# Kernel optimization log

Measured on AMD Instinct MI355X. Metric: run time of the kernel, lower is better.

The kernel has to match this reference:

```python
import jax, jax.numpy as jnp
import numpy as np

N = 1024
IN_F = 256
OUT_F = 128
H = 4
NH = OUT_F // H  # 32
NEG_SLOPE = 0.2


def setup_inputs() -> dict:
    key = jax.random.key(0)
    k1, k2, k3, k4, k5 = jax.random.split(key, 5)
    h = jax.random.normal(k1, (N, IN_F), dtype=jnp.float32)
    adj_mat = jax.random.randint(k2, (N, N, 1), 0, 2, dtype=jnp.int32)
    s_in = 1.0 / np.sqrt(IN_F)
    s_nh = 1.0 / np.sqrt(NH)
    Wl = jax.random.uniform(k3, (H * NH, IN_F), jnp.float32, -s_in, s_in)
    Wr = jax.random.uniform(k4, (H * NH, IN_F), jnp.float32, -s_in, s_in)
    attn_w = jax.random.uniform(k5, (NH,), jnp.float32, -s_nh, s_nh)
    return {"h": h, "adj_mat": adj_mat, "Wl": Wl, "Wr": Wr, "attn_w": attn_w}


def reference(h, adj_mat, Wl, Wr, attn_w):
    n = h.shape[0]
    g_l = (h @ Wl.T).reshape(n, H, NH)  # [N,H,F]
    g_r = (h @ Wr.T).reshape(n, H, NH)  # [N,H,F]
    # g_sum[i, j] = g_l[j] + g_r[i]  (repeat / repeat_interleave semantics)
    g_sum = g_l[None, :, :, :] + g_r[:, None, :, :]  # [N,N,H,F]
    act = jnp.where(g_sum >= 0, g_sum, NEG_SLOPE * g_sum)
    e = jnp.einsum('ijhf,f->ijh', act, attn_w)  # [N,N,H]
    mask = adj_mat != 0  # [N,N,1] broadcasts over heads
    e = jnp.where(mask, e, -jnp.inf)
    a = jax.nn.softmax(e, axis=1)  # softmax over source nodes j
    h_prime = jnp.einsum('ijh,jhf->ihf', a, g_r).reshape(n, H * NH)
    # is_output_layer=False -> ELU (dropout is a no-op in eval)
    return jax.nn.elu(h_prime)
```

## Files before the change

kernel.cpp:

```cpp
#include <hip/hip_runtime.h>
#include <math.h>

#define NN 1024
#define IN_F 256
#define OUT_F 128
#define NHEADS 4
#define NHF 32

__global__ void __launch_bounds__(256) glr_gemm(const float* __restrict__ hmat,
                                                const float* __restrict__ Wl,
                                                const float* __restrict__ Wr,
                                                float* __restrict__ glh,
                                                float* __restrict__ grh) {
    __shared__ float hsh[4][IN_F];
    const int tid = threadIdx.x;
    const int j0  = blockIdx.x * 4;
    for (int t = tid; t < 4 * IN_F; t += 256) {
        hsh[t >> 8][t & 255] = hmat[j0 * IN_F + t];
    }
    __syncthreads();
    const int c = tid;
    const float* __restrict__ Wrow = (c < OUT_F) ? (Wl + c * IN_F) : (Wr + (c - OUT_F) * IN_F);
    float acc0 = 0.f, acc1 = 0.f, acc2 = 0.f, acc3 = 0.f;
#pragma unroll 4
    for (int k = 0; k < IN_F; k += 4) {
        const float4 w  = *(const float4*)(Wrow + k);
        const float4 a0 = *(const float4*)&hsh[0][k];
        const float4 a1 = *(const float4*)&hsh[1][k];
        const float4 a2 = *(const float4*)&hsh[2][k];
        const float4 a3 = *(const float4*)&hsh[3][k];
        acc0 = fmaf(a0.x, w.x, fmaf(a0.y, w.y, fmaf(a0.z, w.z, fmaf(a0.w, w.w, acc0))));
        acc1 = fmaf(a1.x, w.x, fmaf(a1.y, w.y, fmaf(a1.z, w.z, fmaf(a1.w, w.w, acc1))));
        acc2 = fmaf(a2.x, w.x, fmaf(a2.y, w.y, fmaf(a2.z, w.z, fmaf(a2.w, w.w, acc2))));
        acc3 = fmaf(a3.x, w.x, fmaf(a3.y, w.y, fmaf(a3.z, w.z, fmaf(a3.w, w.w, acc3))));
    }
    const int which = (c >= OUT_F);
    const int cc = which ? (c - OUT_F) : c;
    const int hh = cc >> 5, f = cc & 31;
    float* __restrict__ dst = which ? grh : glh;
    dst[(hh * NN + j0 + 0) * NHF + f] = acc0;
    dst[(hh * NN + j0 + 1) * NHF + f] = acc1;
    dst[(hh * NN + j0 + 2) * NHF + f] = acc2;
    dst[(hh * NN + j0 + 3) * NHF + f] = acc3;
}

__global__ void __launch_bounds__(256) gat_main(const float* __restrict__ glh,
                                                const float* __restrict__ grh,
                                                const int* __restrict__ adj,
                                                const float* __restrict__ attn_w,
                                                float* __restrict__ out) {
    const int hh  = blockIdx.y;
    const int i0  = blockIdx.x * 8;
    const int tid = threadIdx.x;

    __shared__ float e_buf[8][1028];
    __shared__ float gr_i[8][32];
    __shared__ float wred[8][4];
    __shared__ float m_sh[8];
    __shared__ float l_sh[8];

    {
        const int ii = tid >> 5, f = tid & 31;
        gr_i[ii][f] = grh[(hh * NN + i0 + ii) * NHF + f];
    }
    float w06[NHF];
#pragma unroll
    for (int f = 0; f < NHF; ++f) w06[f] = 0.6f * attn_w[f];
    const float C23 = 0x1.555556p-1f;
    __syncthreads();

    float mpart[8];
#pragma unroll
    for (int ii = 0; ii < 8; ++ii) mpart[ii] = -1e30f;

    for (int c = 0; c < 4; ++c) {
        const int j = (c << 8) + tid;
        float gl_r[NHF];
#pragma unroll
        for (int f4 = 0; f4 < 8; ++f4) {
            const float4 v = *(const float4*)(glh + (hh * NN + j) * NHF + (f4 << 2));
            gl_r[f4 * 4 + 0] = v.x; gl_r[f4 * 4 + 1] = v.y;
            gl_r[f4 * 4 + 2] = v.z; gl_r[f4 * 4 + 3] = v.w;
        }
        int adjv[8];
#pragma unroll
        for (int ii = 0; ii < 8; ++ii) adjv[ii] = adj[(i0 + ii) * NN + j];
#pragma unroll
        for (int ii = 0; ii < 8; ++ii) {
            float e = 0.f;
#pragma unroll
            for (int f4 = 0; f4 < 8; ++f4) {
                const float4 g = *(const float4*)&gr_i[ii][f4 << 2];
                float s;
                s = gl_r[f4 * 4 + 0] + g.x; e = fmaf(fmaf(fabsf(s), C23, s), w06[f4 * 4 + 0], e);
                s = gl_r[f4 * 4 + 1] + g.y; e = fmaf(fmaf(fabsf(s), C23, s), w06[f4 * 4 + 1], e);
                s = gl_r[f4 * 4 + 2] + g.z; e = fmaf(fmaf(fabsf(s), C23, s), w06[f4 * 4 + 2], e);
                s = gl_r[f4 * 4 + 3] + g.w; e = fmaf(fmaf(fabsf(s), C23, s), w06[f4 * 4 + 3], e);
            }
            e = adjv[ii] ? e : -1e30f;
            e_buf[ii][j] = e;
            mpart[ii] = fmaxf(mpart[ii], e);
        }
    }

#pragma unroll
    for (int ii = 0; ii < 8; ++ii) {
        float v = mpart[ii];
#pragma unroll
        for (int d = 32; d > 0; d >>= 1) v = fmaxf(v, __shfl_xor(v, d));
        if ((tid & 63) == 0) wred[ii][tid >> 6] = v;
    }
    __syncthreads();
    if (tid < 8) m_sh[tid] = fmaxf(fmaxf(wred[tid][0], wred[tid][1]),
                                   fmaxf(wred[tid][2], wred[tid][3]));
    __syncthreads();

    float lpart[8];
#pragma unroll
    for (int ii = 0; ii < 8; ++ii) lpart[ii] = 0.f;
    for (int c = 0; c < 4; ++c) {
        const int j = (c << 8) + tid;
#pragma unroll
        for (int ii = 0; ii < 8; ++ii) {
            const float p = __expf(e_buf[ii][j] - m_sh[ii]);
            e_buf[ii][j] = p;
            lpart[ii] += p;
        }
    }
#pragma unroll
    for (int ii = 0; ii < 8; ++ii) {
        float v = lpart[ii];
#pragma unroll
        for (int d = 32; d > 0; d >>= 1) v += __shfl_xor(v, d);
        if ((tid & 63) == 0) wred[ii][tid >> 6] = v;
    }
    __syncthreads();
    if (tid < 8) l_sh[tid] = wred[tid][0] + wred[tid][1] + wred[tid][2] + wred[tid][3];
    __syncthreads();

    const int ii = tid >> 5, f = tid & 31;
    const float* __restrict__ grb = grh + hh * NN * NHF + f;
    float o0 = 0.f, o1 = 0.f, o2 = 0.f, o3 = 0.f;
    for (int j = 0; j < NN; j += 4) {
        const float4 p4 = *(const float4*)&e_buf[ii][j];
        const float g0 = grb[(j + 0) * NHF];
        const float g1 = grb[(j + 1) * NHF];
        const float g2 = grb[(j + 2) * NHF];
        const float g3 = grb[(j + 3) * NHF];
        o0 = fmaf(p4.x, g0, o0);
        o1 = fmaf(p4.y, g1, o1);
        o2 = fmaf(p4.z, g2, o2);
        o3 = fmaf(p4.w, g3, o3);
    }
    float o = (o0 + o1) + (o2 + o3);
    o /= l_sh[ii];
    const float r = (o > 0.f) ? o : (__expf(o) - 1.f);
    out[(i0 + ii) * OUT_F + hh * NHF + f] = r;
}

extern "C" void kernel_launch(void* const* d_in, const int* in_sizes, int n_in,
                              void* d_out, int out_size, void* d_ws, size_t ws_size,
                              hipStream_t stream) {
    const float* hmat = (const float*)d_in[0];
    const int*   adj  = (const int*)d_in[1];
    const float* Wl   = (const float*)d_in[2];
    const float* Wr   = (const float*)d_in[3];
    const float* aw   = (const float*)d_in[4];
    float* o          = (float*)d_out;

    float* glh = (float*)d_ws;
    float* grh = glh + NHEADS * NN * NHF;

    glr_gemm<<<dim3(NN / 4), dim3(256), 0, stream>>>(hmat, Wl, Wr, glh, grh);
    gat_main<<<dim3(NN / 8, NHEADS), dim3(256), 0, stream>>>(glh, grh, adj, aw, o);
}
```

Measured before the change: 122.0 us.

## Split LeakyReLU into linear dot terms plus abs term, widen blocks and restructure aggregation

Leaky ReLU is rewritten as 0.6*s + 0.4*|s|, so the linear part of the attention score becomes per-node dot products (alpha, beta). These are computed in the GEMM kernel with a warp shuffle reduction, which leaves one abs-FMA per feature in the main loop. The main kernel moves to 512 threads. Aggregation now splits the j range across thread groups, each accumulating all 8 rows, then reduces partials in shared memory, which reuses each grh load for 8 rows. The GEMM processes 2 rows per block instead of 4, which doubles weight reloads, and the extra shared buffer may reduce occupancy.

```diff
diff --git a/kernel.cpp b/kernel.cpp
--- a/kernel.cpp
+++ b/kernel.cpp
@@ -10,116 +10,125 @@
 __global__ void __launch_bounds__(256) glr_gemm(const float* __restrict__ hmat,
                                                 const float* __restrict__ Wl,
                                                 const float* __restrict__ Wr,
+                                                const float* __restrict__ attn_w,
                                                 float* __restrict__ glh,
-                                                float* __restrict__ grh) {
-    __shared__ float hsh[4][IN_F];
+                                                float* __restrict__ grh,
+                                                float* __restrict__ alpha,
+                                                float* __restrict__ beta) {
+    __shared__ float hsh[2][IN_F];
     const int tid = threadIdx.x;
-    const int j0  = blockIdx.x * 4;
-    for (int t = tid; t < 4 * IN_F; t += 256) {
+    const int j0  = blockIdx.x * 2;
+    for (int t = tid; t < 2 * IN_F; t += 256) {
         hsh[t >> 8][t & 255] = hmat[j0 * IN_F + t];
     }
     __syncthreads();
     const int c = tid;
     const float* __restrict__ Wrow = (c < OUT_F) ? (Wl + c * IN_F) : (Wr + (c - OUT_F) * IN_F);
-    float acc0 = 0.f, acc1 = 0.f, acc2 = 0.f, acc3 = 0.f;
-#pragma unroll 4
+    float a0 = 0.f, a1 = 0.f;
+#pragma unroll 8
     for (int k = 0; k < IN_F; k += 4) {
         const float4 w  = *(const float4*)(Wrow + k);
-        const float4 a0 = *(const float4*)&hsh[0][k];
-        const float4 a1 = *(const float4*)&hsh[1][k];
-        const float4 a2 = *(const float4*)&hsh[2][k];
-        const float4 a3 = *(const float4*)&hsh[3][k];
-        acc0 = fmaf(a0.x, w.x, fmaf(a0.y, w.y, fmaf(a0.z, w.z, fmaf(a0.w, w.w, acc0))));
-        acc1 = fmaf(a1.x, w.x, fmaf(a1.y, w.y, fmaf(a1.z, w.z, fmaf(a1.w, w.w, acc1))));
-        acc2 = fmaf(a2.x, w.x, fmaf(a2.y, w.y, fmaf(a2.z, w.z, fmaf(a2.w, w.w, acc2))));
-        acc3 = fmaf(a3.x, w.x, fmaf(a3.y, w.y, fmaf(a3.z, w.z, fmaf(a3.w, w.w, acc3))));
+        const float4 x0 = *(const float4*)&hsh[0][k];
+        const float4 x1 = *(const float4*)&hsh[1][k];
+        a0 = fmaf(x0.x, w.x, fmaf(x0.y, w.y, fmaf(x0.z, w.z, fmaf(x0.w, w.w, a0))));
+        a1 = fmaf(x1.x, w.x, fmaf(x1.y, w.y, fmaf(x1.z, w.z, fmaf(x1.w, w.w, a1))));
+    }
+    const int f = c & 31;
+    const float wf = attn_w[f];
+    float d0 = a0 * wf, d1 = a1 * wf;
+#pragma unroll
+    for (int d = 16; d > 0; d >>= 1) {
+        d0 += __shfl_xor(d0, d);
+        d1 += __shfl_xor(d1, d);
     }
     const int which = (c >= OUT_F);
     const int cc = which ? (c - OUT_F) : c;
-    const int hh = cc >> 5, f = cc & 31;
+    const int hh = cc >> 5;
     float* __restrict__ dst = which ? grh : glh;
-    dst[(hh * NN + j0 + 0) * NHF + f] = acc0;
-    dst[(hh * NN + j0 + 1) * NHF + f] = acc1;
-    dst[(hh * NN + j0 + 2) * NHF + f] = acc2;
-    dst[(hh * NN + j0 + 3) * NHF + f] = acc3;
+    dst[(hh * NN + j0 + 0) * NHF + f] = a0;
+    dst[(hh * NN + j0 + 1) * NHF + f] = a1;
+    if (f == 0) {
+        float* __restrict__ ab = which ? beta : alpha;
+        ab[hh * NN + j0 + 0] = d0;
+        ab[hh * NN + j0 + 1] = d1;
+    }
 }
 
-__global__ void __launch_bounds__(256) gat_main(const float* __restrict__ glh,
-                                                const float* __restrict__ grh,
-                                                const int* __restrict__ adj,
-                                                const float* __restrict__ attn_w,
-                                                float* __restrict__ out) {
+__global__ void __launch_bounds__(512, 4) gat_main(const float* __restrict__ glh,
+                                                   const float* __restrict__ grh,
+                                                   const float* __restrict__ alpha,
+                                                   const float* __restrict__ beta,
+                                                   const int* __restrict__ adj,
+                                                   const float* __restrict__ attn_w,
+                                                   float* __restrict__ out) {
     const int hh  = blockIdx.y;
     const int i0  = blockIdx.x * 8;
     const int tid = threadIdx.x;
 
     __shared__ float e_buf[8][1028];
-    __shared__ float gr_i[8][32];
-    __shared__ float wred[8][4];
-    __shared__ float m_sh[8];
-    __shared__ float l_sh[8];
-
-    {
-        const int ii = tid >> 5, f = tid & 31;
-        gr_i[ii][f] = grh[(hh * NN + i0 + ii) * NHF + f];
-    }
-    float w06[NHF];
-#pragma unroll
-    for (int f = 0; f < NHF; ++f) w06[f] = 0.6f * attn_w[f];
-    const float C23 = 0x1.555556p-1f;
-    __syncthreads();
+    __shared__ float part[8][16][32];
+    __shared__ float red[8][8];
+    __shared__ float m_sh[8], l_sh[8];
 
     float mpart[8];
 #pragma unroll
     for (int ii = 0; ii < 8; ++ii) mpart[ii] = -1e30f;
 
-    for (int c = 0; c < 4; ++c) {
-        const int j = (c << 8) + tid;
-        float gl_r[NHF];
+    for (int c = 0; c < 2; ++c) {
+        const int j = (c << 9) + tid;
+        const float* __restrict__ gp = glh + (hh * NN + j) * NHF;
+        float gl[32];
 #pragma unroll
         for (int f4 = 0; f4 < 8; ++f4) {
-            const float4 v = *(const float4*)(glh + (hh * NN + j) * NHF + (f4 << 2));
-            gl_r[f4 * 4 + 0] = v.x; gl_r[f4 * 4 + 1] = v.y;
-            gl_r[f4 * 4 + 2] = v.z; gl_r[f4 * 4 + 3] = v.w;
-        }
+            const float4 v = *(const float4*)(gp + (f4 << 2));
+            gl[f4 * 4 + 0] = v.x; gl[f4 * 4 + 1] = v.y;
+            gl[f4 * 4 + 2] = v.z; gl[f4 * 4 + 3] = v.w;
+        }
+        const float aj = alpha[hh * NN + j];
         int adjv[8];
 #pragma unroll
         for (int ii = 0; ii < 8; ++ii) adjv[ii] = adj[(i0 + ii) * NN + j];
 #pragma unroll
         for (int ii = 0; ii < 8; ++ii) {
-            float e = 0.f;
-#pragma unroll
-            for (int f4 = 0; f4 < 8; ++f4) {
-                const float4 g = *(const float4*)&gr_i[ii][f4 << 2];
-                float s;
-                s = gl_r[f4 * 4 + 0] + g.x; e = fmaf(fmaf(fabsf(s), C23, s), w06[f4 * 4 + 0], e);
-                s = gl_r[f4 * 4 + 1] + g.y; e = fmaf(fmaf(fabsf(s), C23, s), w06[f4 * 4 + 1], e);
-                s = gl_r[f4 * 4 + 2] + g.z; e = fmaf(fmaf(fabsf(s), C23, s), w06[f4 * 4 + 2], e);
-                s = gl_r[f4 * 4 + 3] + g.w; e = fmaf(fmaf(fabsf(s), C23, s), w06[f4 * 4 + 3], e);
+            const float* __restrict__ grp = grh + (hh * NN + i0 + ii) * NHF;
+            float S0 = 0.f, S1 = 0.f;
+#pragma unroll
+            for (int f = 0; f < 32; f += 2) {
+                const float s0 = gl[f]     + grp[f];
+                const float s1 = gl[f + 1] + grp[f + 1];
+                S0 = fmaf(fabsf(s0), attn_w[f],     S0);
+                S1 = fmaf(fabsf(s1), attn_w[f + 1], S1);
             }
+            const float bi = beta[hh * NN + i0 + ii];
+            float e = fmaf(0.4f, S0 + S1, 0.6f * (aj + bi));
             e = adjv[ii] ? e : -1e30f;
             e_buf[ii][j] = e;
             mpart[ii] = fmaxf(mpart[ii], e);
         }
     }
 
+    const int lane = tid & 63, wv = tid >> 6;
 #pragma unroll
     for (int ii = 0; ii < 8; ++ii) {
         float v = mpart[ii];
 #pragma unroll
         for (int d = 32; d > 0; d >>= 1) v = fmaxf(v, __shfl_xor(v, d));
-        if ((tid & 63) == 0) wred[ii][tid >> 6] = v;
-    }
-    __syncthreads();
-    if (tid < 8) m_sh[tid] = fmaxf(fmaxf(wred[tid][0], wred[tid][1]),
-                                   fmaxf(wred[tid][2], wred[tid][3]));
+        if (lane == 0) red[ii][wv] = v;
+    }
+    __syncthreads();
+    if (tid < 8) {
+        float m = red[tid][0];
+#pragma unroll
+        for (int w = 1; w < 8; ++w) m = fmaxf(m, red[tid][w]);
+        m_sh[tid] = m;
+    }
     __syncthreads();
 
     float lpart[8];
 #pragma unroll
     for (int ii = 0; ii < 8; ++ii) lpart[ii] = 0.f;
-    for (int c = 0; c < 4; ++c) {
-        const int j = (c << 8) + tid;
+    for (int c = 0; c < 2; ++c) {
+        const int j = (c << 9) + tid;
 #pragma unroll
         for (int ii = 0; ii < 8; ++ii) {
             const float p = __expf(e_buf[ii][j] - m_sh[ii]);
@@ -132,30 +141,49 @@
         float v = lpart[ii];
 #pragma unroll
         for (int d = 32; d > 0; d >>= 1) v += __shfl_xor(v, d);
-        if ((tid & 63) == 0) wred[ii][tid >> 6] = v;
-    }
-    __syncthreads();
-    if (tid < 8) l_sh[tid] = wred[tid][0] + wred[tid][1] + wred[tid][2] + wred[tid][3];
-    __syncthreads();
-
-    const int ii = tid >> 5, f = tid & 31;
-    const float* __restrict__ grb = grh + hh * NN * NHF + f;
-    float o0 = 0.f, o1 = 0.f, o2 = 0.f, o3 = 0.f;
-    for (int j = 0; j < NN; j += 4) {
-        const float4 p4 = *(const float4*)&e_buf[ii][j];
-        const float g0 = grb[(j + 0) * NHF];
-        const float g1 = grb[(j + 1) * NHF];
-        const float g2 = grb[(j + 2) * NHF];
-        const float g3 = grb[(j + 3) * NHF];
-        o0 = fmaf(p4.x, g0, o0);
-        o1 = fmaf(p4.y, g1, o1);
-        o2 = fmaf(p4.z, g2, o2);
-        o3 = fmaf(p4.w, g3, o3);
-    }
-    float o = (o0 + o1) + (o2 + o3);
-    o /= l_sh[ii];
-    const float r = (o > 0.f) ? o : (__expf(o) - 1.f);
-    out[(i0 + ii) * OUT_F + hh * NHF + f] = r;
+        if (lane == 0) red[ii][wv] = v;
+    }
+    __syncthreads();
+    if (tid < 8) {
+        float l = red[tid][0];
+#pragma unroll
+        for (int w = 1; w < 8; ++w) l += red[tid][w];
+        l_sh[tid] = l;
+    }
+    __syncthreads();
+
+    const int f  = tid & 31;
+    const int js = tid >> 5;
+    const float* __restrict__ gp = grh + hh * NN * NHF + f;
+    float o[8];
+#pragma unroll
+    for (int ii = 0; ii < 8; ++ii) o[ii] = 0.f;
+    const int jbase = js << 6;
+    for (int jj = 0; jj < 64; jj += 4) {
+        const int j = jbase + jj;
+        const float g0 = gp[(j + 0) * NHF];
+        const float g1 = gp[(j + 1) * NHF];
+        const float g2 = gp[(j + 2) * NHF];
+        const float g3 = gp[(j + 3) * NHF];
+#pragma unroll
+        for (int ii = 0; ii < 8; ++ii) {
+            const float4 p4 = *(const float4*)&e_buf[ii][j];
+            o[ii] = fmaf(p4.x, g0, fmaf(p4.y, g1, fmaf(p4.z, g2, fmaf(p4.w, g3, o[ii]))));
+        }
+    }
+#pragma unroll
+    for (int ii = 0; ii < 8; ++ii) part[ii][js][f] = o[ii];
+    __syncthreads();
+
+    if (tid < 256) {
+        const int ii = tid >> 5, ff = tid & 31;
+        float s = 0.f;
+#pragma unroll
+        for (int k = 0; k < 16; ++k) s += part[ii][k][ff];
+        s /= l_sh[ii];
+        const float r = (s > 0.f) ? s : (__expf(s) - 1.f);
+        out[(i0 + ii) * OUT_F + hh * NHF + ff] = r;
+    }
 }
 
 extern "C" void kernel_launch(void* const* d_in, const int* in_sizes, int n_in,
@@ -168,9 +196,11 @@
     const float* aw   = (const float*)d_in[4];
     float* o          = (float*)d_out;
 
-    float* glh = (float*)d_ws;
-    float* grh = glh + NHEADS * NN * NHF;
-
-    glr_gemm<<<dim3(NN / 4), dim3(256), 0, stream>>>(hmat, Wl, Wr, glh, grh);
-    gat_main<<<dim3(NN / 8, NHEADS), dim3(256), 0, stream>>>(glh, grh, adj, aw, o);
+    float* glh   = (float*)d_ws;
+    float* grh   = glh + NHEADS * NN * NHF;
+    float* alpha = grh + NHEADS * NN * NHF;
+    float* beta  = alpha + NHEADS * NN;
+
+    glr_gemm<<<dim3(NN / 2), dim3(256), 0, stream>>>(hmat, Wl, Wr, aw, glh, grh, alpha, beta);
+    gat_main<<<dim3(NN / 8, NHEADS), dim3(512), 0, stream>>>(glh, grh, alpha, beta, adj, aw, o);
 }
```

After: 108.9 us. 10.7% less time.
